# Kernel optimization log

Measured on AMD Instinct MI355X. Metric: run time of the kernel, lower is better.

Reference implementation:

```python
import jax, jax.numpy as jnp
import numpy as np

N_NODES = 100000
N_EDGES = 1600000
IN_C, HID_C, OUT_C, N_CLS = 64, 128, 64, 20


def setup_inputs() -> dict:
    key = jax.random.key(0)
    ks = jax.random.split(key, 8)
    s = lambda k, sh: jax.random.normal(k, sh, dtype=jnp.float32) * (1.0 / np.sqrt(sh[0]))
    return {
        "x": jax.random.normal(ks[0], (N_NODES, IN_C), dtype=jnp.float32),
        "edge_index": jax.random.randint(ks[1], (2, N_EDGES), 0, N_NODES, dtype=jnp.int64),
        "w_self1": s(ks[2], (IN_C, HID_C)),
        "w_neigh1": s(ks[3], (IN_C, HID_C)),
        "b1": jnp.zeros((HID_C,), dtype=jnp.float32),
        "w_self2": s(ks[4], (HID_C, OUT_C)),
        "w_neigh2": s(ks[5], (HID_C, OUT_C)),
        "b2": jnp.zeros((OUT_C,), dtype=jnp.float32),
        "wc": s(ks[6], (OUT_C, N_CLS)),
        "bc": jnp.zeros((N_CLS,), dtype=jnp.float32),
    }


def _sage_mean(feat, src, dst, deg_inv, w_self, w_neigh, b):
    # gather messages along edges, segment-sum at destinations, mean-normalize
    msg_sum = jax.ops.segment_sum(feat[src], dst, num_segments=N_NODES)  # [N, d]
    h_neigh = msg_sum * deg_inv[:, None]
    return feat @ w_self + h_neigh @ w_neigh + b


def reference(x, edge_index, w_self1, w_neigh1, b1, w_self2, w_neigh2, b2, wc, bc):
    src, dst = edge_index[0], edge_index[1]
    deg = jax.ops.segment_sum(jnp.ones((src.shape[0],), dtype=x.dtype), dst,
                              num_segments=N_NODES)
    deg_inv = 1.0 / jnp.maximum(deg, 1.0)  # zero-degree nodes -> 0 neighbor mean
    h = jax.nn.relu(_sage_mean(x, src, dst, deg_inv, w_self1, w_neigh1, b1))
    h = jax.nn.relu(_sage_mean(h, src, dst, deg_inv, w_self2, w_neigh2, b2))
    return h @ wc + bc
```

## Files before the change

### kernel.cpp

```cpp
#include <hip/hip_runtime.h>

#define N_NODES 100000
#define N_EDGES 1600000
#define IN_C    64
#define HID_C   128
#define OUT_C   64
#define N_CLS   20

#define BUCKETS 196
#define XSL     8
#define WCAP    2560
#define EPB     4096
#define CAPB    44

#define CVT_BLOCKS 3125

typedef __attribute__((ext_vector_type(8))) short short8;
typedef __attribute__((ext_vector_type(4))) float floatx4;

__device__ __forceinline__ unsigned short f2bf(float f) {
    union { float f; unsigned u; } v; v.f = f;
    unsigned r = v.u + 0x7FFFu + ((v.u >> 16) & 1u);
    return (unsigned short)(r >> 16);
}
__device__ __forceinline__ unsigned pk2(float lo, float hi) {
    return (unsigned)f2bf(lo) | ((unsigned)f2bf(hi) << 16);
}
__device__ __forceinline__ float bflo(unsigned w) { return __uint_as_float(w << 16); }
__device__ __forceinline__ float bfhi(unsigned w) { return __uint_as_float(w & 0xFFFF0000u); }

#define ACC8(v) do { \
    a0 += bflo((v).x); a1 += bfhi((v).x); a2 += bflo((v).y); a3 += bfhi((v).y); \
    a4 += bflo((v).z); a5 += bfhi((v).z); a6 += bflo((v).w); a7 += bfhi((v).w); } while (0)

__global__ __launch_bounds__(256) void prologue_kernel(
        const float* __restrict__ x,
        const float* __restrict__ ws1, const float* __restrict__ wn1,
        const float* __restrict__ ws2, const float* __restrict__ wn2,
        unsigned short* __restrict__ xb,
        unsigned short* __restrict__ wt1s, unsigned short* __restrict__ wt1n,
        unsigned short* __restrict__ wt2s, unsigned short* __restrict__ wt2n,
        int* __restrict__ bcnt)
{
    const int bid = blockIdx.x, tid = threadIdx.x;
    if (bid < CVT_BLOCKS) {
        int i = bid * 256 + tid;
        float4 a = ((const float4*)x)[(size_t)i * 2];
        float4 b = ((const float4*)x)[(size_t)i * 2 + 1];
        uint4 r;
        r.x = pk2(a.x, a.y); r.y = pk2(a.z, a.w);
        r.z = pk2(b.x, b.y); r.w = pk2(b.z, b.w);
        ((uint4*)xb)[i] = r;
    } else if (bid == CVT_BLOCKS) {
        for (int i = tid; i < BUCKETS * XSL; i += 256) bcnt[i] = 0;
    } else {
        int i = (bid - CVT_BLOCKS - 1) * 256 + tid;
        if (i < 8192) {
            int o = i >> 6, c = i & 63;
            wt1s[i] = f2bf(ws1[c * 128 + o]);
            wt1n[i] = f2bf(wn1[c * 128 + o]);
        } else if (i < 16384) {
            int j = i - 8192;
            int o = j >> 7, c = j & 127;
            wt2s[j] = f2bf(ws2[c * 64 + o]);
            wt2n[j] = f2bf(wn2[c * 64 + o]);
        }
    }
}

__global__ __launch_bounds__(256) void binA_kernel(
        const int* __restrict__ ei, int* __restrict__ bcnt,
        unsigned* __restrict__ bins)
{
    __shared__ unsigned lbins[BUCKETS * CAPB];
    __shared__ unsigned comp[EPB];
    __shared__ unsigned dsti[EPB];
    __shared__ int lcnt[BUCKETS], lofs[BUCKETS], gb[BUCKETS];
    __shared__ int sd[256];

    const int tid = threadIdx.x;
    const int xcd = blockIdx.x & (XSL - 1);
    const int e0  = blockIdx.x * EPB;

    for (int w = tid; w < BUCKETS; w += 256) lcnt[w] = 0;
    __syncthreads();

    for (int it = 0; it < EPB / 256; ++it) {
        int e = e0 + it * 256 + tid;
        if (e >= N_EDGES) break;
        int src = ei[e];
        int dst = ei[N_EDGES + e];
        int b = dst >> 9;
        unsigned pk = ((unsigned)(dst & 511) << 17) | (unsigned)src;
        int pos = atomicAdd(&lcnt[b], 1);
        if (pos < CAPB) {
            lbins[b * CAPB + pos] = pk;
        } else {
            int gp = atomicAdd(&bcnt[b * XSL + xcd], 1);
            if (gp < WCAP)
                bins[(unsigned)(b * XSL + xcd) * WCAP + gp] = pk;
        }
    }
    __syncthreads();

    int c = (tid < BUCKETS) ? min(lcnt[tid], CAPB) : 0;
    sd[tid] = c;
    __syncthreads();
    for (int off = 1; off < 256; off <<= 1) {
        int x = 0;
        if (tid >= off) x = sd[tid - off];
        __syncthreads();
        if (tid >= off) sd[tid] += x;
        __syncthreads();
    }
    if (tid < BUCKETS) lofs[tid] = sd[tid] - c;
    __syncthreads();
    const int T = sd[255];

    if (tid < BUCKETS) {
        int cw = min(lcnt[tid], CAPB);
        gb[tid] = (cw > 0) ? atomicAdd(&bcnt[tid * XSL + xcd], cw) : 0;
    }
    __syncthreads();

    if (tid < BUCKETS) {
        int cw = min(lcnt[tid], CAPB);
        int lo = lofs[tid];
        unsigned wb = (unsigned)(tid * XSL + xcd) * WCAP + (unsigned)gb[tid];
        for (int i = 0; i < cw; ++i) {
            comp[lo + i] = lbins[tid * CAPB + i];
            dsti[lo + i] = wb + i;
        }
    }
    __syncthreads();

    for (int i = tid; i < T; i += 256)
        bins[dsti[i]] = comp[i];
}

__global__ __launch_bounds__(256) void buildB_kernel(
        const int* __restrict__ bcnt, const unsigned* __restrict__ bins,
        int* __restrict__ row_ptr, int* __restrict__ sorted_src,
        float* __restrict__ dinv)
{
    __shared__ unsigned ent[16384];
    __shared__ int scnt[XSL], soff[XSL];
    __shared__ int cnt[512], lofs[512], cur[512];
    __shared__ int sd[256];
    __shared__ int gbase_s;

    const int b   = blockIdx.x;
    const int tid = threadIdx.x;
    const int node0 = b * 512;

    int part = 0;
    for (int w = tid; w < b * XSL; w += 256) part += min(bcnt[w], WCAP);
    sd[tid] = part;
    __syncthreads();
    for (int off = 128; off > 0; off >>= 1) {
        if (tid < off) sd[tid] += sd[tid + off];
        __syncthreads();
    }
    if (tid == 0) {
        gbase_s = sd[0];
        if (b == 0) row_ptr[N_NODES] = N_EDGES;
    }
    __syncthreads();

    if (tid < XSL) scnt[tid] = min(bcnt[b * XSL + tid], WCAP);
    { int i = tid; cnt[i] = 0; cnt[i + 256] = 0; }
    __syncthreads();
    if (tid == 0) {
        int acc = 0;
        for (int sl = 0; sl < XSL; ++sl) {
            soff[sl] = acc;
            acc += scnt[sl];
            if (acc > 16384) { scnt[sl] -= (acc - 16384); acc = 16384; }
        }
    }
    __syncthreads();

    for (int sl = 0; sl < XSL; ++sl) {
        int len = scnt[sl];
        const unsigned* seg = bins + (unsigned)(b * XSL + sl) * WCAP;
        int base = soff[sl];
        for (int i = tid; i < len; i += 256) {
            unsigned e = seg[i];
            ent[base + i] = e;
            atomicAdd((unsigned*)&cnt[e >> 17], 1u);
        }
    }
    __syncthreads();
    const int T = soff[XSL - 1] + scnt[XSL - 1];

    int a0 = cnt[2 * tid], a1 = cnt[2 * tid + 1];
    int s2 = a0 + a1;
    sd[tid] = s2;
    __syncthreads();
    for (int off = 1; off < 256; off <<= 1) {
        int x = 0;
        if (tid >= off) x = sd[tid - off];
        __syncthreads();
        if (tid >= off) sd[tid] += x;
        __syncthreads();
    }
    int excl = sd[tid] - s2;
    lofs[2 * tid]     = excl;
    lofs[2 * tid + 1] = excl + a0;
    cur[2 * tid]      = excl;
    cur[2 * tid + 1]  = excl + a0;
    __syncthreads();

    const int gbase = gbase_s;
    for (int j = tid; j < 512; j += 256) {
        int node = node0 + j;
        if (node < N_NODES) {
            row_ptr[node] = gbase + lofs[j];
            dinv[node] = 1.0f / (float)max(cnt[j], 1);
        }
    }
    for (int i = tid; i < T; i += 256) {
        unsigned e = ent[i];
        int dl = e >> 17;
        int p = atomicAdd((unsigned*)&cur[dl], 1u);
        sorted_src[gbase + p] = (int)(e & 0x1FFFFu);
    }
}

__global__ __launch_bounds__(256, 8) void fused1_kernel(
        const int* __restrict__ row_ptr, const int* __restrict__ srcs,
        const unsigned short* __restrict__ xb,
        const float* __restrict__ dinv,
        const unsigned short* __restrict__ wt1s,
        const unsigned short* __restrict__ wt1n,
        const float* __restrict__ b1,
        const unsigned short* __restrict__ wt2n,
        const unsigned short* __restrict__ wt2s,
        const float* __restrict__ b2,
        unsigned short* __restrict__ t2b,
        unsigned short* __restrict__ s2b)
{
    __shared__ unsigned short sbuf[32 * 136];

    const int tid = threadIdx.x;
    const int node0 = blockIdx.x * 32;

    {
        const int q  = tid & 7;
        const int np = tid >> 3;
        const int n = node0 + np;
        const uint4* f4 = (const uint4*)xb;
        float a0=0,a1=0,a2=0,a3=0,a4=0,a5=0,a6=0,a7=0;
        int beg = row_ptr[n];
        int end = row_ptr[n + 1];
        int e = beg;
        for (; e + 4 <= end; e += 4) {
            int s0 = srcs[e], s1 = srcs[e+1], s2 = srcs[e+2], s3 = srcs[e+3];
            uint4 v0 = f4[(size_t)s0 * 8 + q];
            uint4 v1 = f4[(size_t)s1 * 8 + q];
            uint4 v2 = f4[(size_t)s2 * 8 + q];
            uint4 v3 = f4[(size_t)s3 * 8 + q];
            ACC8(v0); ACC8(v1); ACC8(v2); ACC8(v3);
        }
        for (; e < end; ++e) {
            uint4 v = f4[(size_t)srcs[e] * 8 + q];
            ACC8(v);
        }
        float di = dinv[n];
        a0*=di; a1*=di; a2*=di; a3*=di; a4*=di; a5*=di; a6*=di; a7*=di;
        uint4 r;
        r.x = pk2(a0, a1); r.y = pk2(a2, a3);
        r.z = pk2(a4, a5); r.w = pk2(a6, a7);
        *(uint4*)(sbuf + np * 72 + q * 8) = r;
    }
    __syncthreads();

    const int lane  = tid & 63;
    const int wv    = tid >> 6;
    const int quad  = lane >> 4;
    const int col   = lane & 15;
    const int nrow  = (wv & 1) * 16 + col;
    const int mhalf = wv >> 1;
    const int nl = node0 + nrow;

    {
        const short8 bs0 = *(const short8*)(xb + (size_t)nl * 64 +      quad * 8);
        const short8 bs1 = *(const short8*)(xb + (size_t)nl * 64 + 32 + quad * 8);
        const short8 bn0 = *(const short8*)(sbuf + nrow * 72 +      quad * 8);
        const short8 bn1 = *(const short8*)(sbuf + nrow * 72 + 32 + quad * 8);
        __syncthreads();

#pragma unroll
        for (int mt = 0; mt < 4; ++mt) {
            int mb = mhalf * 4 + mt;
            int m = mb * 16 + col;
            const short8 as0 = *(const short8*)(wt1s + (size_t)m * 64 +      quad * 8);
            const short8 as1 = *(const short8*)(wt1s + (size_t)m * 64 + 32 + quad * 8);
            const short8 an0 = *(const short8*)(wt1n + (size_t)m * 64 +      quad * 8);
            const short8 an1 = *(const short8*)(wt1n + (size_t)m * 64 + 32 + quad * 8);
            floatx4 acc = {0.f, 0.f, 0.f, 0.f};
            acc = __builtin_amdgcn_mfma_f32_16x16x32_bf16(as0, bs0, acc, 0, 0, 0);
            acc = __builtin_amdgcn_mfma_f32_16x16x32_bf16(as1, bs1, acc, 0, 0, 0);
            acc = __builtin_amdgcn_mfma_f32_16x16x32_bf16(an0, bn0, acc, 0, 0, 0);
            acc = __builtin_amdgcn_mfma_f32_16x16x32_bf16(an1, bn1, acc, 0, 0, 0);
            int och = mb * 16 + quad * 4;
            float4 bv = *(const float4*)(b1 + och);
            ushort4 r;
            r.x = f2bf(fmaxf(acc[0] + bv.x, 0.f));
            r.y = f2bf(fmaxf(acc[1] + bv.y, 0.f));
            r.z = f2bf(fmaxf(acc[2] + bv.z, 0.f));
            r.w = f2bf(fmaxf(acc[3] + bv.w, 0.f));
            *(ushort4*)(sbuf + nrow * 136 + och) = r;
        }
    }
    __syncthreads();

    {
        short8 bfr[4];
#pragma unroll
        for (int kc = 0; kc < 4; ++kc)
            bfr[kc] = *(const short8*)(sbuf + nrow * 136 + kc * 32 + quad * 8);

#pragma unroll
        for (int mt = 0; mt < 2; ++mt) {
            int mb = mhalf * 2 + mt;
            int m = mb * 16 + col;
            floatx4 at = {0.f, 0.f, 0.f, 0.f};
            floatx4 as = {0.f, 0.f, 0.f, 0.f};
#pragma unroll
            for (int kc = 0; kc < 4; ++kc) {
                const short8 an = *(const short8*)(wt2n + (size_t)m * 128 + kc * 32 + quad * 8);
                const short8 aw = *(const short8*)(wt2s + (size_t)m * 128 + kc * 32 + quad * 8);
                at = __builtin_amdgcn_mfma_f32_16x16x32_bf16(an, bfr[kc], at, 0, 0, 0);
                as = __builtin_amdgcn_mfma_f32_16x16x32_bf16(aw, bfr[kc], as, 0, 0, 0);
            }
            int och = mb * 16 + quad * 4;
            ushort4 rt;
            rt.x = f2bf(at[0]); rt.y = f2bf(at[1]);
            rt.z = f2bf(at[2]); rt.w = f2bf(at[3]);
            *(ushort4*)(t2b + (size_t)nl * 64 + och) = rt;
            float4 bv = *(const float4*)(b2 + och);
            ushort4 rs;
            rs.x = f2bf(as[0] + bv.x); rs.y = f2bf(as[1] + bv.y);
            rs.z = f2bf(as[2] + bv.z); rs.w = f2bf(as[3] + bv.w);
            *(ushort4*)(s2b + (size_t)nl * 64 + och) = rs;
        }
    }
}

__global__ __launch_bounds__(256, 8) void fused2_kernel(
        const int* __restrict__ row_ptr, const int* __restrict__ srcs,
        const unsigned short* __restrict__ t2b,
        const unsigned short* __restrict__ s2b,
        const float* __restrict__ dinv,
        const float* __restrict__ wc,
        const float* __restrict__ bc,
        float* __restrict__ out)
{
    __shared__ float hs[32][68];

    const int tid = threadIdx.x;
    const int node0 = blockIdx.x * 32;

    {
        const int q  = tid & 7;
        const int np = tid >> 3;
        const int n = node0 + np;
        const uint4* f4 = (const uint4*)t2b;
        float a0=0,a1=0,a2=0,a3=0,a4=0,a5=0,a6=0,a7=0;
        int beg = row_ptr[n];
        int end = row_ptr[n + 1];
        int e = beg;
        for (; e + 4 <= end; e += 4) {
            int s0 = srcs[e], s1 = srcs[e+1], s2 = srcs[e+2], s3 = srcs[e+3];
            uint4 v0 = f4[(size_t)s0 * 8 + q];
            uint4 v1 = f4[(size_t)s1 * 8 + q];
            uint4 v2 = f4[(size_t)s2 * 8 + q];
            uint4 v3 = f4[(size_t)s3 * 8 + q];
            ACC8(v0); ACC8(v1); ACC8(v2); ACC8(v3);
        }
        for (; e < end; ++e) {
            uint4 v = f4[(size_t)srcs[e] * 8 + q];
            ACC8(v);
        }
        float di = dinv[n];
        uint4 sv = *(const uint4*)(s2b + (size_t)n * 64 + q * 8);
        float* d = hs[np] + q * 8;
        d[0] = fmaxf(a0 * di + bflo(sv.x), 0.f);
        d[1] = fmaxf(a1 * di + bfhi(sv.x), 0.f);
        d[2] = fmaxf(a2 * di + bflo(sv.y), 0.f);
        d[3] = fmaxf(a3 * di + bfhi(sv.y), 0.f);
        d[4] = fmaxf(a4 * di + bflo(sv.z), 0.f);
        d[5] = fmaxf(a5 * di + bfhi(sv.z), 0.f);
        d[6] = fmaxf(a6 * di + bflo(sv.w), 0.f);
        d[7] = fmaxf(a7 * di + bfhi(sv.w), 0.f);
    }
    __syncthreads();

    for (int o = tid; o < 32 * N_CLS; o += 256) {
        int n = o / N_CLS, cls = o % N_CLS;
        float s = bc[cls];
#pragma unroll
        for (int k = 0; k < 64; ++k) s += hs[n][k] * wc[k * N_CLS + cls];
        out[(size_t)(node0 + n) * N_CLS + cls] = s;
    }
}


extern "C" void kernel_launch(void* const* d_in, const int* in_sizes, int n_in,
                              void* d_out, int out_size, void* d_ws, size_t ws_size,
                              hipStream_t stream)
{
    const float* x        = (const float*)d_in[0];
    const int*   ei       = (const int*)  d_in[1];
    const float* w_self1  = (const float*)d_in[2];
    const float* w_neigh1 = (const float*)d_in[3];
    const float* b1       = (const float*)d_in[4];
    const float* w_self2  = (const float*)d_in[5];
    const float* w_neigh2 = (const float*)d_in[6];
    const float* b2       = (const float*)d_in[7];
    const float* wc       = (const float*)d_in[8];
    const float* bc       = (const float*)d_in[9];
    float* out = (float*)d_out;

    const size_t N = N_NODES;
    int*      bcnt    = (int*)d_ws;
    int*      row_ptr = bcnt + BUCKETS * XSL + 8;
    unsigned* bins    = (unsigned*)(row_ptr + N + 8);
    int*      s_src   = (int*)(bins + BUCKETS * XSL * WCAP);
    float*    dinv    = (float*)(s_src + N_EDGES);
    unsigned short* xb    = (unsigned short*)(dinv + N);
    unsigned short* t2b   = xb + 64 * N;
    unsigned short* s2b   = t2b + 64 * N;
    unsigned short* wt1s  = s2b + 64 * N;
    unsigned short* wt1n  = wt1s + 8192;
    unsigned short* wt2s  = wt1n + 8192;
    unsigned short* wt2n  = wt2s + 8192;

    const int PB  = CVT_BLOCKS + 1 + 64;
    const int EB2 = (N_EDGES + EPB - 1) / EPB;
    const int MB32 = (N_NODES + 31) / 32;

    prologue_kernel<<<PB, 256, 0, stream>>>(x, w_self1, w_neigh1, w_self2,
                                            w_neigh2, xb, wt1s, wt1n, wt2s,
                                            wt2n, bcnt);
    binA_kernel<<<EB2, 256, 0, stream>>>(ei, bcnt, bins);
    buildB_kernel<<<BUCKETS, 256, 0, stream>>>(bcnt, bins, row_ptr, s_src, dinv);
    fused1_kernel<<<MB32, 256, 0, stream>>>(row_ptr, s_src, xb, dinv,
                                            wt1s, wt1n, b1, wt2n, wt2s, b2,
                                            t2b, s2b);
    fused2_kernel<<<MB32, 256, 0, stream>>>(row_ptr, s_src, t2b, s2b, dinv,
                                            wc, bc, out);
}
```

Before: 284.4 us.

## Split layer-1 gather out of fused MLP kernel into separate kernel

Splits the layer-1 neighbor aggregation out of the fused gather+MFMA kernel into its own gather kernel. That kernel writes the mean-aggregated bf16 features to a new global buffer, and a separate MLP kernel reads them back. The intent is to decouple the latency-bound gather from the MFMA stage, with its own occupancy settings, and to remove block-level syncs. In exchange it adds an extra kernel launch and a 12.8MB write plus read-back of the intermediate aggregate.

```diff
diff --git a/kernel.cpp b/kernel.cpp
--- a/kernel.cpp
+++ b/kernel.cpp
@@ -227,10 +227,43 @@
     }
 }
 
-__global__ __launch_bounds__(256, 8) void fused1_kernel(
+__global__ __launch_bounds__(256) void gather1_kernel(
         const int* __restrict__ row_ptr, const int* __restrict__ srcs,
+        const unsigned short* __restrict__ featb,
+        const float* __restrict__ dinv, unsigned short* __restrict__ aggb)
+{
+    int gid = blockIdx.x * 256 + threadIdx.x;
+    int n = gid >> 3;
+    int q = gid & 7;
+    const uint4* f4 = (const uint4*)featb;
+    float a0=0,a1=0,a2=0,a3=0,a4=0,a5=0,a6=0,a7=0;
+    int beg = row_ptr[n];
+    int end = row_ptr[n + 1];
+    int e = beg;
+    for (; e + 4 <= end; e += 4) {
+        int s0 = srcs[e], s1 = srcs[e+1], s2 = srcs[e+2], s3 = srcs[e+3];
+        uint4 v0 = f4[(size_t)s0 * 8 + q];
+        uint4 v1 = f4[(size_t)s1 * 8 + q];
+        uint4 v2 = f4[(size_t)s2 * 8 + q];
+        uint4 v3 = f4[(size_t)s3 * 8 + q];
+        ACC8(v0); ACC8(v1); ACC8(v2); ACC8(v3);
+    }
+    for (; e < end; ++e) {
+        uint4 v = f4[(size_t)srcs[e] * 8 + q];
+        ACC8(v);
+    }
+    float di = dinv[n];
+    uint4 r;
+    r.x = pk2(a0 * di, a1 * di);
+    r.y = pk2(a2 * di, a3 * di);
+    r.z = pk2(a4 * di, a5 * di);
+    r.w = pk2(a6 * di, a7 * di);
+    ((uint4*)aggb)[(size_t)n * 8 + q] = r;
+}
+
+__global__ __launch_bounds__(256, 8) void mlp1_kernel(
         const unsigned short* __restrict__ xb,
-        const float* __restrict__ dinv,
+        const unsigned short* __restrict__ aggb,
         const unsigned short* __restrict__ wt1s,
         const unsigned short* __restrict__ wt1n,
         const float* __restrict__ b1,
@@ -245,36 +278,6 @@
     const int tid = threadIdx.x;
     const int node0 = blockIdx.x * 32;
 
-    {
-        const int q  = tid & 7;
-        const int np = tid >> 3;
-        const int n = node0 + np;
-        const uint4* f4 = (const uint4*)xb;
-        float a0=0,a1=0,a2=0,a3=0,a4=0,a5=0,a6=0,a7=0;
-        int beg = row_ptr[n];
-        int end = row_ptr[n + 1];
-        int e = beg;
-        for (; e + 4 <= end; e += 4) {
-            int s0 = srcs[e], s1 = srcs[e+1], s2 = srcs[e+2], s3 = srcs[e+3];
-            uint4 v0 = f4[(size_t)s0 * 8 + q];
-            uint4 v1 = f4[(size_t)s1 * 8 + q];
-            uint4 v2 = f4[(size_t)s2 * 8 + q];
-            uint4 v3 = f4[(size_t)s3 * 8 + q];
-            ACC8(v0); ACC8(v1); ACC8(v2); ACC8(v3);
-        }
-        for (; e < end; ++e) {
-            uint4 v = f4[(size_t)srcs[e] * 8 + q];
-            ACC8(v);
-        }
-        float di = dinv[n];
-        a0*=di; a1*=di; a2*=di; a3*=di; a4*=di; a5*=di; a6*=di; a7*=di;
-        uint4 r;
-        r.x = pk2(a0, a1); r.y = pk2(a2, a3);
-        r.z = pk2(a4, a5); r.w = pk2(a6, a7);
-        *(uint4*)(sbuf + np * 72 + q * 8) = r;
-    }
-    __syncthreads();
-
     const int lane  = tid & 63;
     const int wv    = tid >> 6;
     const int quad  = lane >> 4;
@@ -284,11 +287,10 @@
     const int nl = node0 + nrow;
 
     {
-        const short8 bs0 = *(const short8*)(xb + (size_t)nl * 64 +      quad * 8);
-        const short8 bs1 = *(const short8*)(xb + (size_t)nl * 64 + 32 + quad * 8);
-        const short8 bn0 = *(const short8*)(sbuf + nrow * 72 +      quad * 8);
-        const short8 bn1 = *(const short8*)(sbuf + nrow * 72 + 32 + quad * 8);
-        __syncthreads();
+        const short8 bs0 = *(const short8*)(xb   + (size_t)nl * 64 +      quad * 8);
+        const short8 bs1 = *(const short8*)(xb   + (size_t)nl * 64 + 32 + quad * 8);
+        const short8 bn0 = *(const short8*)(aggb + (size_t)nl * 64 +      quad * 8);
+        const short8 bn1 = *(const short8*)(aggb + (size_t)nl * 64 + 32 + quad * 8);
 
 #pragma unroll
         for (int mt = 0; mt < 4; ++mt) {
@@ -430,7 +432,8 @@
     int*      s_src   = (int*)(bins + BUCKETS * XSL * WCAP);
     float*    dinv    = (float*)(s_src + N_EDGES);
     unsigned short* xb    = (unsigned short*)(dinv + N);
-    unsigned short* t2b   = xb + 64 * N;
+    unsigned short* agg1b = xb + 64 * N;
+    unsigned short* t2b   = agg1b + 64 * N;
     unsigned short* s2b   = t2b + 64 * N;
     unsigned short* wt1s  = s2b + 64 * N;
     unsigned short* wt1n  = wt1s + 8192;
@@ -439,6 +442,7 @@
 
     const int PB  = CVT_BLOCKS + 1 + 64;
     const int EB2 = (N_EDGES + EPB - 1) / EPB;
+    const int GB  = (N_NODES * 8) / 256;
     const int MB32 = (N_NODES + 31) / 32;
 
     prologue_kernel<<<PB, 256, 0, stream>>>(x, w_self1, w_neigh1, w_self2,
@@ -446,9 +450,9 @@
                                             wt2n, bcnt);
     binA_kernel<<<EB2, 256, 0, stream>>>(ei, bcnt, bins);
     buildB_kernel<<<BUCKETS, 256, 0, stream>>>(bcnt, bins, row_ptr, s_src, dinv);
-    fused1_kernel<<<MB32, 256, 0, stream>>>(row_ptr, s_src, xb, dinv,
-                                            wt1s, wt1n, b1, wt2n, wt2s, b2,
-                                            t2b, s2b);
+    gather1_kernel<<<GB, 256, 0, stream>>>(row_ptr, s_src, xb, dinv, agg1b);
+    mlp1_kernel<<<MB32, 256, 0, stream>>>(xb, agg1b, wt1s, wt1n, b1,
+                                          wt2n, wt2s, b2, t2b, s2b);
     fused2_kernel<<<MB32, 256, 0, stream>>>(row_ptr, s_src, t2b, s2b, dinv,
                                             wc, bc, out);
 }
```

Measured after the change: 305.5 us. +7.4%, slower.
